# Optimization experiments

Measured on AMD Instinct MI355X. Metric: run time of the kernel, lower is better.

The kernel has to match this reference:

```python
import jax, jax.numpy as jnp
import numpy as np


def setup_inputs() -> dict:
    key = jax.random.key(0)
    k0, k1, k2, k3 = jax.random.split(key, 4)
    U, I, D, E = 100000, 50000, 128, 300000
    user_emb = jax.random.normal(k0, (U, D), dtype=jnp.float32) * 0.1
    item_emb = jax.random.normal(k1, (I, D), dtype=jnp.float32) * 0.1
    ui_src = jax.random.randint(k2, (E,), 0, U)          # user ids
    ui_dst = jax.random.randint(k3, (E,), 0, I)          # item ids
    # reverse ('item','rev_rates','user') edges are the transpose of the rating edges
    iu_src = ui_dst
    iu_dst = ui_src
    return {
        "user_emb": user_emb,
        "item_emb": item_emb,
        "ui_src": ui_src,
        "ui_dst": ui_dst,
        "iu_src": iu_src,
        "iu_dst": iu_dst,
        "num_users": U,
        "num_items": I,
        "num_layers": 2,
    }


def reference(user_emb, item_emb, ui_src, ui_dst, iu_src, iu_dst,
              num_users, num_items, num_layers):
    # Build homogeneous graph: item ids offset by num_users (as in encode()).
    N = num_users + num_items
    src = jnp.concatenate([ui_src, iu_src + num_users])        # [2E]
    dst = jnp.concatenate([ui_dst + num_users, iu_dst])        # [2E]
    x = jnp.concatenate([user_emb, item_emb], axis=0)          # [N, D]

    # gcn_norm without self-loops (PyG LGConv default): deg from in-edges.
    ones = jnp.ones(src.shape, dtype=x.dtype)
    deg = jax.ops.segment_sum(ones, dst, num_segments=N)       # [N]
    deg_inv_sqrt = jnp.where(deg > 0, 1.0 / jnp.sqrt(jnp.maximum(deg, 1.0)), 0.0)
    norm = deg_inv_sqrt[src] * deg_inv_sqrt[dst]               # [2E]

    # LightGCN: propagate num_layers times, average all layer outputs
    # (dropout is identity in eval mode).
    acc = x
    for _ in range(num_layers):
        x = jax.ops.segment_sum(x[src] * norm[:, None], dst, num_segments=N)
        acc = acc + x
    final = acc / (num_layers + 1)
    return final[:num_users], final[num_users:]
```

## Files before the change

kernel.cpp:

```cpp
#include <hip/hip_runtime.h>
#include <hip/hip_bf16.h>


#define DIM 128

struct __align__(8) Pair { int s; float w; };

__device__ __forceinline__ ushort f2bf(float f) {
    uint u = __float_as_uint(f);
    u += 0x7fffu + ((u >> 16) & 1u);
    return (ushort)(u >> 16);
}
__device__ __forceinline__ float bflo(uint u) { return __uint_as_float(u << 16); }
__device__ __forceinline__ float bfhi(uint u) { return __uint_as_float(u & 0xffff0000u); }

__global__ void deg_kernel(const int* __restrict__ ui_dst,
                           const int* __restrict__ iu_dst,
                           int E, int U, int* __restrict__ deg) {
    int e = blockIdx.x * blockDim.x + threadIdx.x;
    if (e < E) {
        atomicAdd(&deg[ui_dst[e] + U], 1);
        atomicAdd(&deg[iu_dst[e]], 1);
    }
}

__device__ __forceinline__ int block_incl_scan(int v, int* lds) {
    int lane = threadIdx.x & 63;
    int wid = threadIdx.x >> 6;
    int nw = (blockDim.x + 63) >> 6;
    #pragma unroll
    for (int off = 1; off < 64; off <<= 1) {
        int t = __shfl_up(v, off);
        if (lane >= off) v += t;
    }
    if (lane == 63) lds[wid] = v;
    __syncthreads();
    if (threadIdx.x == 0) {
        int s = 0;
        for (int w = 0; w < nw; w++) { int t = lds[w]; lds[w] = s; s += t; }
    }
    __syncthreads();
    return v + lds[wid];
}

__global__ void scan_partial_kernel(const int* __restrict__ deg, int N,
                                    int* __restrict__ partials) {
    __shared__ int lds[16];
    int i = blockIdx.x * 256 + threadIdx.x;
    int v = (i < N) ? deg[i] : 0;
    int incl = block_incl_scan(v, lds);
    if (threadIdx.x == 255) partials[blockIdx.x] = incl;
}

__global__ void scan_top_kernel(int* __restrict__ partials, int P,
                                int* __restrict__ row_ptr, int N) {
    __shared__ int lds[16];
    int i = threadIdx.x;
    int v = (i < P) ? partials[i] : 0;
    int incl = block_incl_scan(v, lds);
    if (i < P) partials[i] = incl - v;
    if (i == (int)blockDim.x - 1) row_ptr[N] = incl;
}

__global__ void scan_final_kernel(const int* __restrict__ deg, int N,
                                  const int* __restrict__ partials,
                                  int* __restrict__ row_ptr,
                                  int* __restrict__ cursor,
                                  float* __restrict__ dinv) {
    __shared__ int lds[16];
    int i = blockIdx.x * 256 + threadIdx.x;
    int v = (i < N) ? deg[i] : 0;
    int incl = block_incl_scan(v, lds);
    if (i < N) {
        int excl = incl - v + partials[blockIdx.x];
        row_ptr[i] = excl;
        cursor[i] = excl;
        dinv[i] = (v > 0) ? (1.0f / sqrtf((float)v)) : 0.0f;
    }
}

__global__ void fill_kernel(const int* __restrict__ ui_src,
                            const int* __restrict__ ui_dst,
                            const int* __restrict__ iu_src,
                            const int* __restrict__ iu_dst,
                            const float* __restrict__ dinv,
                            int E, int U,
                            int* __restrict__ cursor, Pair* __restrict__ pairs) {
    int e = blockIdx.x * blockDim.x + threadIdx.x;
    if (e >= E) return;
    int s = ui_src[e], d = ui_dst[e] + U;
    int pos = atomicAdd(&cursor[d], 1);
    pairs[pos] = {s, dinv[s]};
    s = iu_src[e] + U; d = iu_dst[e];
    pos = atomicAdd(&cursor[d], 1);
    pairs[pos] = {s, dinv[s]};
}

__global__ void convert_kernel(const float* __restrict__ xu,
                               const float* __restrict__ xi,
                               long uelems, long total,
                               ushort* __restrict__ xb) {
    long i8 = ((long)blockIdx.x * blockDim.x + threadIdx.x) * 8;
    if (i8 >= total) return;
    const float* src = (i8 < uelems) ? (xu + i8) : (xi + (i8 - uelems));
    float4 a = *reinterpret_cast<const float4*>(src);
    float4 b = *reinterpret_cast<const float4*>(src + 4);
    uint4 q;
    q.x = ((uint)f2bf(a.y) << 16) | f2bf(a.x);
    q.y = ((uint)f2bf(a.w) << 16) | f2bf(a.z);
    q.z = ((uint)f2bf(b.y) << 16) | f2bf(b.x);
    q.w = ((uint)f2bf(b.w) << 16) | f2bf(b.z);
    *reinterpret_cast<uint4*>(xb + i8) = q;
}

__global__ __launch_bounds__(256) void gather1_kernel(
        const ushort* __restrict__ xb,
        const int* __restrict__ row_ptr, const Pair* __restrict__ pairs,
        const float* __restrict__ dinv, int N, ushort* __restrict__ Tb) {
    long gt = (long)blockIdx.x * blockDim.x + threadIdx.x;
    int lane = (int)(gt & 15);
    long node = gt >> 4;
    if (node >= N) return;
    int start = row_ptr[node], end = row_ptr[node + 1];
    float a0 = 0.f, a1 = 0.f, a2 = 0.f, a3 = 0.f, a4 = 0.f, a5 = 0.f, a6 = 0.f, a7 = 0.f;
    int j = start;
    for (; j + 2 <= end; j += 2) {
        Pair p0 = pairs[j], p1 = pairs[j + 1];
        uint4 q0 = *reinterpret_cast<const uint4*>(xb + (size_t)p0.s * DIM + lane * 8);
        uint4 q1 = *reinterpret_cast<const uint4*>(xb + (size_t)p1.s * DIM + lane * 8);
        a0 = fmaf(bflo(q0.x), p0.w, fmaf(bflo(q1.x), p1.w, a0));
        a1 = fmaf(bfhi(q0.x), p0.w, fmaf(bfhi(q1.x), p1.w, a1));
        a2 = fmaf(bflo(q0.y), p0.w, fmaf(bflo(q1.y), p1.w, a2));
        a3 = fmaf(bfhi(q0.y), p0.w, fmaf(bfhi(q1.y), p1.w, a3));
        a4 = fmaf(bflo(q0.z), p0.w, fmaf(bflo(q1.z), p1.w, a4));
        a5 = fmaf(bfhi(q0.z), p0.w, fmaf(bfhi(q1.z), p1.w, a5));
        a6 = fmaf(bflo(q0.w), p0.w, fmaf(bflo(q1.w), p1.w, a6));
        a7 = fmaf(bfhi(q0.w), p0.w, fmaf(bfhi(q1.w), p1.w, a7));
    }
    if (j < end) {
        Pair p = pairs[j];
        uint4 q = *reinterpret_cast<const uint4*>(xb + (size_t)p.s * DIM + lane * 8);
        a0 = fmaf(bflo(q.x), p.w, a0);
        a1 = fmaf(bfhi(q.x), p.w, a1);
        a2 = fmaf(bflo(q.y), p.w, a2);
        a3 = fmaf(bfhi(q.y), p.w, a3);
        a4 = fmaf(bflo(q.z), p.w, a4);
        a5 = fmaf(bfhi(q.z), p.w, a5);
        a6 = fmaf(bflo(q.w), p.w, a6);
        a7 = fmaf(bfhi(q.w), p.w, a7);
    }
    float dd = dinv[node];
    uint4 r;
    r.x = ((uint)f2bf(a1 * dd) << 16) | f2bf(a0 * dd);
    r.y = ((uint)f2bf(a3 * dd) << 16) | f2bf(a2 * dd);
    r.z = ((uint)f2bf(a5 * dd) << 16) | f2bf(a4 * dd);
    r.w = ((uint)f2bf(a7 * dd) << 16) | f2bf(a6 * dd);
    *reinterpret_cast<uint4*>(Tb + (size_t)node * DIM + lane * 8) = r;
}

__global__ __launch_bounds__(256) void gather2_kernel(
        const float* __restrict__ xu, const float* __restrict__ xi,
        const ushort* __restrict__ Tb,
        const int* __restrict__ row_ptr, const Pair* __restrict__ pairs,
        const float* __restrict__ dinv, int N, int U, float* __restrict__ out) {
    long gt = (long)blockIdx.x * blockDim.x + threadIdx.x;
    int lane = (int)(gt & 15);
    long node = gt >> 4;
    if (node >= N) return;
    int start = row_ptr[node], end = row_ptr[node + 1];
    float a0 = 0.f, a1 = 0.f, a2 = 0.f, a3 = 0.f, a4 = 0.f, a5 = 0.f, a6 = 0.f, a7 = 0.f;
    int j = start;
    for (; j + 2 <= end; j += 2) {
        Pair p0 = pairs[j], p1 = pairs[j + 1];
        uint4 q0 = *reinterpret_cast<const uint4*>(Tb + (size_t)p0.s * DIM + lane * 8);
        uint4 q1 = *reinterpret_cast<const uint4*>(Tb + (size_t)p1.s * DIM + lane * 8);
        a0 = fmaf(bflo(q0.x), p0.w, fmaf(bflo(q1.x), p1.w, a0));
        a1 = fmaf(bfhi(q0.x), p0.w, fmaf(bfhi(q1.x), p1.w, a1));
        a2 = fmaf(bflo(q0.y), p0.w, fmaf(bflo(q1.y), p1.w, a2));
        a3 = fmaf(bfhi(q0.y), p0.w, fmaf(bfhi(q1.y), p1.w, a3));
        a4 = fmaf(bflo(q0.z), p0.w, fmaf(bflo(q1.z), p1.w, a4));
        a5 = fmaf(bfhi(q0.z), p0.w, fmaf(bfhi(q1.z), p1.w, a5));
        a6 = fmaf(bflo(q0.w), p0.w, fmaf(bflo(q1.w), p1.w, a6));
        a7 = fmaf(bfhi(q0.w), p0.w, fmaf(bfhi(q1.w), p1.w, a7));
    }
    if (j < end) {
        Pair p = pairs[j];
        uint4 q = *reinterpret_cast<const uint4*>(Tb + (size_t)p.s * DIM + lane * 8);
        a0 = fmaf(bflo(q.x), p.w, a0);
        a1 = fmaf(bfhi(q.x), p.w, a1);
        a2 = fmaf(bflo(q.y), p.w, a2);
        a3 = fmaf(bfhi(q.y), p.w, a3);
        a4 = fmaf(bflo(q.z), p.w, a4);
        a5 = fmaf(bfhi(q.z), p.w, a5);
        a6 = fmaf(bflo(q.w), p.w, a6);
        a7 = fmaf(bfhi(q.w), p.w, a7);
    }
    float dd = dinv[node];
    size_t off = (size_t)node * DIM + lane * 8;
    uint4 tq = *reinterpret_cast<const uint4*>(Tb + off);
    const float* x0p = (node < (long)U) ? (xu + off) : (xi + off - (size_t)U * DIM);
    float4 xa = *reinterpret_cast<const float4*>(x0p);
    float4 xc = *reinterpret_cast<const float4*>(x0p + 4);
    const float k = 1.0f / 3.0f;
    float4 r0, r1;
    r0.x = (xa.x + bflo(tq.x) + a0 * dd) * k;
    r0.y = (xa.y + bfhi(tq.x) + a1 * dd) * k;
    r0.z = (xa.z + bflo(tq.y) + a2 * dd) * k;
    r0.w = (xa.w + bfhi(tq.y) + a3 * dd) * k;
    r1.x = (xc.x + bflo(tq.z) + a4 * dd) * k;
    r1.y = (xc.y + bfhi(tq.z) + a5 * dd) * k;
    r1.z = (xc.z + bflo(tq.w) + a6 * dd) * k;
    r1.w = (xc.w + bfhi(tq.w) + a7 * dd) * k;
    *reinterpret_cast<float4*>(out + off) = r0;
    *reinterpret_cast<float4*>(out + off + 4) = r1;
}

extern "C" void kernel_launch(void* const* d_in, const int* in_sizes, int n_in,
                              void* d_out, int out_size, void* d_ws, size_t ws_size,
                              hipStream_t stream) {
    const float* user_emb = (const float*)d_in[0];
    const float* item_emb = (const float*)d_in[1];
    const int* ui_src = (const int*)d_in[2];
    const int* ui_dst = (const int*)d_in[3];
    const int* iu_src = (const int*)d_in[4];
    const int* iu_dst = (const int*)d_in[5];

    const int E = in_sizes[2];
    const int U = in_sizes[0] / DIM;
    const int I = in_sizes[1] / DIM;
    const int N = U + I;
    const int twoE = 2 * E;
    const long uelems = (long)U * DIM;
    const long total = (long)N * DIM;

    float* out = (float*)d_out;

    char* ws = (char*)d_ws;
    size_t off = 0;
    int* deg = (int*)(ws + off); off += (size_t)N * 4;
    int* cursor = (int*)(ws + off); off += (size_t)N * 4;
    int* row_ptr = (int*)(ws + off); off += (size_t)(N + 1) * 4;
    int* partials = (int*)(ws + off); off += 1024 * 4;
    float* dinv = (float*)(ws + off); off += (size_t)N * 4;
    off = (off + 7) & ~(size_t)7;
    Pair* pairs = (Pair*)(ws + off); off += (size_t)twoE * 8;
    off = (off + 511) & ~(size_t)511;
    ushort* xb = (ushort*)(ws + off); off += (size_t)total * 2;
    off = (off + 511) & ~(size_t)511;
    ushort* Tb = (ushort*)(ws + off);

    const int nPartBlocks = (N + 255) / 256;

    hipMemsetAsync(deg, 0, (size_t)N * 4, stream);

    deg_kernel<<<(E + 255) / 256, 256, 0, stream>>>(ui_dst, iu_dst, E, U, deg);

    scan_partial_kernel<<<nPartBlocks, 256, 0, stream>>>(deg, N, partials);
    scan_top_kernel<<<1, 1024, 0, stream>>>(partials, nPartBlocks, row_ptr, N);
    scan_final_kernel<<<nPartBlocks, 256, 0, stream>>>(deg, N, partials,
                                                       row_ptr, cursor, dinv);

    fill_kernel<<<(E + 255) / 256, 256, 0, stream>>>(ui_src, ui_dst, iu_src, iu_dst,
                                                     dinv, E, U, cursor, pairs);

    {
        long cthreads = total / 8;
        int cblocks = (int)((cthreads + 255) / 256);
        convert_kernel<<<cblocks, 256, 0, stream>>>(user_emb, item_emb,
                                                    uelems, total, xb);
    }

    {
        long threads = (long)N * 16;
        int blocks = (int)((threads + 255) / 256);
        gather1_kernel<<<blocks, 256, 0, stream>>>(xb, row_ptr, pairs, dinv, N, Tb);
        gather2_kernel<<<blocks, 256, 0, stream>>>(user_emb, item_emb, Tb,
                                                   row_ptr, pairs, dinv, N, U, out);
    }
}
```

Measured before the change: 292.4 us.

## Fuse all LightGCN stages into one cooperative persistent kernel with grid syncs

```diff
diff --git a/kernel.cpp b/kernel.cpp
--- a/kernel.cpp
+++ b/kernel.cpp
@@ -1,8 +1,13 @@
 #include <hip/hip_runtime.h>
+#include <hip/hip_cooperative_groups.h>
 #include <hip/hip_bf16.h>
 
+namespace cg = cooperative_groups;
+
 
 #define DIM 128
+#define NBLOCKS 1024
+#define NTHR 256
 
 struct __align__(8) Pair { int s; float w; };
 
@@ -14,20 +19,9 @@
 __device__ __forceinline__ float bflo(uint u) { return __uint_as_float(u << 16); }
 __device__ __forceinline__ float bfhi(uint u) { return __uint_as_float(u & 0xffff0000u); }
 
-__global__ void deg_kernel(const int* __restrict__ ui_dst,
-                           const int* __restrict__ iu_dst,
-                           int E, int U, int* __restrict__ deg) {
-    int e = blockIdx.x * blockDim.x + threadIdx.x;
-    if (e < E) {
-        atomicAdd(&deg[ui_dst[e] + U], 1);
-        atomicAdd(&deg[iu_dst[e]], 1);
-    }
-}
-
 __device__ __forceinline__ int block_incl_scan(int v, int* lds) {
     int lane = threadIdx.x & 63;
     int wid = threadIdx.x >> 6;
-    int nw = (blockDim.x + 63) >> 6;
     #pragma unroll
     for (int off = 1; off < 64; off <<= 1) {
         int t = __shfl_up(v, off);
@@ -37,200 +31,210 @@
     __syncthreads();
     if (threadIdx.x == 0) {
         int s = 0;
-        for (int w = 0; w < nw; w++) { int t = lds[w]; lds[w] = s; s += t; }
+        #pragma unroll
+        for (int w = 0; w < 4; w++) { int t = lds[w]; lds[w] = s; s += t; }
     }
     __syncthreads();
     return v + lds[wid];
 }
 
-__global__ void scan_partial_kernel(const int* __restrict__ deg, int N,
-                                    int* __restrict__ partials) {
+__global__ __launch_bounds__(256, 4) void lightgcn_all(
+        const float* __restrict__ xu, const float* __restrict__ xi,
+        const int* __restrict__ ui_src, const int* __restrict__ ui_dst,
+        const int* __restrict__ iu_src, const int* __restrict__ iu_dst,
+        int E, int U, int I,
+        int* __restrict__ deg, int* __restrict__ cursor,
+        int* __restrict__ row_ptr, int* __restrict__ partials,
+        float* __restrict__ dinv, Pair* __restrict__ pairs,
+        ushort* __restrict__ xb, ushort* __restrict__ Tb,
+        float* __restrict__ out) {
+    cg::grid_group grid = cg::this_grid();
     __shared__ int lds[16];
-    int i = blockIdx.x * 256 + threadIdx.x;
-    int v = (i < N) ? deg[i] : 0;
-    int incl = block_incl_scan(v, lds);
-    if (threadIdx.x == 255) partials[blockIdx.x] = incl;
-}
-
-__global__ void scan_top_kernel(int* __restrict__ partials, int P,
-                                int* __restrict__ row_ptr, int N) {
-    __shared__ int lds[16];
-    int i = threadIdx.x;
-    int v = (i < P) ? partials[i] : 0;
-    int incl = block_incl_scan(v, lds);
-    if (i < P) partials[i] = incl - v;
-    if (i == (int)blockDim.x - 1) row_ptr[N] = incl;
-}
-
-__global__ void scan_final_kernel(const int* __restrict__ deg, int N,
-                                  const int* __restrict__ partials,
-                                  int* __restrict__ row_ptr,
-                                  int* __restrict__ cursor,
-                                  float* __restrict__ dinv) {
-    __shared__ int lds[16];
-    int i = blockIdx.x * 256 + threadIdx.x;
-    int v = (i < N) ? deg[i] : 0;
-    int incl = block_incl_scan(v, lds);
-    if (i < N) {
-        int excl = incl - v + partials[blockIdx.x];
+    __shared__ int runsh;
+
+    const int N = U + I;
+    const long tid = (long)blockIdx.x * blockDim.x + threadIdx.x;
+    const long nth = (long)gridDim.x * blockDim.x;
+    const long total = (long)N * DIM;
+    const long uelems = (long)U * DIM;
+
+    for (long i = tid; i < N; i += nth) deg[i] = 0;
+    grid.sync();
+
+    for (long e = tid; e < E; e += nth) {
+        atomicAdd(&deg[ui_dst[e] + U], 1);
+        atomicAdd(&deg[iu_dst[e]], 1);
+    }
+    for (long u = tid; u < (total >> 3); u += nth) {
+        long i8 = u << 3;
+        const float* src = (i8 < uelems) ? (xu + i8) : (xi + (i8 - uelems));
+        float4 a = *reinterpret_cast<const float4*>(src);
+        float4 b = *reinterpret_cast<const float4*>(src + 4);
+        uint4 q;
+        q.x = ((uint)f2bf(a.y) << 16) | f2bf(a.x);
+        q.y = ((uint)f2bf(a.w) << 16) | f2bf(a.z);
+        q.z = ((uint)f2bf(b.y) << 16) | f2bf(b.x);
+        q.w = ((uint)f2bf(b.w) << 16) | f2bf(b.z);
+        *reinterpret_cast<uint4*>(xb + i8) = q;
+    }
+    grid.sync();
+
+    const int nchunk = (N + 255) >> 8;
+    for (int c = blockIdx.x; c < nchunk; c += gridDim.x) {
+        int i = (c << 8) + threadIdx.x;
+        int v = (i < N) ? deg[i] : 0;
+        int incl = block_incl_scan(v, lds);
+        if (i < N) row_ptr[i] = incl - v;
+        if (threadIdx.x == 255) partials[c] = incl;
+        __syncthreads();
+    }
+    grid.sync();
+
+    if (blockIdx.x == 0) {
+        if (threadIdx.x == 0) runsh = 0;
+        __syncthreads();
+        for (int base = 0; base < nchunk; base += 256) {
+            int idx = base + threadIdx.x;
+            int v = (idx < nchunk) ? partials[idx] : 0;
+            int incl = block_incl_scan(v, lds);
+            int run = runsh;
+            __syncthreads();
+            if (idx < nchunk) partials[idx] = incl - v + run;
+            if (threadIdx.x == 255) runsh = run + incl;
+            __syncthreads();
+        }
+        if (threadIdx.x == 0) row_ptr[N] = runsh;
+    }
+    grid.sync();
+
+    for (long i = tid; i < N; i += nth) {
+        int excl = row_ptr[i] + partials[i >> 8];
         row_ptr[i] = excl;
         cursor[i] = excl;
-        dinv[i] = (v > 0) ? (1.0f / sqrtf((float)v)) : 0.0f;
-    }
-}
-
-__global__ void fill_kernel(const int* __restrict__ ui_src,
-                            const int* __restrict__ ui_dst,
-                            const int* __restrict__ iu_src,
-                            const int* __restrict__ iu_dst,
-                            const float* __restrict__ dinv,
-                            int E, int U,
-                            int* __restrict__ cursor, Pair* __restrict__ pairs) {
-    int e = blockIdx.x * blockDim.x + threadIdx.x;
-    if (e >= E) return;
-    int s = ui_src[e], d = ui_dst[e] + U;
-    int pos = atomicAdd(&cursor[d], 1);
-    pairs[pos] = {s, dinv[s]};
-    s = iu_src[e] + U; d = iu_dst[e];
-    pos = atomicAdd(&cursor[d], 1);
-    pairs[pos] = {s, dinv[s]};
-}
-
-__global__ void convert_kernel(const float* __restrict__ xu,
-                               const float* __restrict__ xi,
-                               long uelems, long total,
-                               ushort* __restrict__ xb) {
-    long i8 = ((long)blockIdx.x * blockDim.x + threadIdx.x) * 8;
-    if (i8 >= total) return;
-    const float* src = (i8 < uelems) ? (xu + i8) : (xi + (i8 - uelems));
-    float4 a = *reinterpret_cast<const float4*>(src);
-    float4 b = *reinterpret_cast<const float4*>(src + 4);
-    uint4 q;
-    q.x = ((uint)f2bf(a.y) << 16) | f2bf(a.x);
-    q.y = ((uint)f2bf(a.w) << 16) | f2bf(a.z);
-    q.z = ((uint)f2bf(b.y) << 16) | f2bf(b.x);
-    q.w = ((uint)f2bf(b.w) << 16) | f2bf(b.z);
-    *reinterpret_cast<uint4*>(xb + i8) = q;
-}
-
-__global__ __launch_bounds__(256) void gather1_kernel(
-        const ushort* __restrict__ xb,
-        const int* __restrict__ row_ptr, const Pair* __restrict__ pairs,
-        const float* __restrict__ dinv, int N, ushort* __restrict__ Tb) {
-    long gt = (long)blockIdx.x * blockDim.x + threadIdx.x;
-    int lane = (int)(gt & 15);
-    long node = gt >> 4;
-    if (node >= N) return;
-    int start = row_ptr[node], end = row_ptr[node + 1];
-    float a0 = 0.f, a1 = 0.f, a2 = 0.f, a3 = 0.f, a4 = 0.f, a5 = 0.f, a6 = 0.f, a7 = 0.f;
-    int j = start;
-    for (; j + 2 <= end; j += 2) {
-        Pair p0 = pairs[j], p1 = pairs[j + 1];
-        uint4 q0 = *reinterpret_cast<const uint4*>(xb + (size_t)p0.s * DIM + lane * 8);
-        uint4 q1 = *reinterpret_cast<const uint4*>(xb + (size_t)p1.s * DIM + lane * 8);
-        a0 = fmaf(bflo(q0.x), p0.w, fmaf(bflo(q1.x), p1.w, a0));
-        a1 = fmaf(bfhi(q0.x), p0.w, fmaf(bfhi(q1.x), p1.w, a1));
-        a2 = fmaf(bflo(q0.y), p0.w, fmaf(bflo(q1.y), p1.w, a2));
-        a3 = fmaf(bfhi(q0.y), p0.w, fmaf(bfhi(q1.y), p1.w, a3));
-        a4 = fmaf(bflo(q0.z), p0.w, fmaf(bflo(q1.z), p1.w, a4));
-        a5 = fmaf(bfhi(q0.z), p0.w, fmaf(bfhi(q1.z), p1.w, a5));
-        a6 = fmaf(bflo(q0.w), p0.w, fmaf(bflo(q1.w), p1.w, a6));
-        a7 = fmaf(bfhi(q0.w), p0.w, fmaf(bfhi(q1.w), p1.w, a7));
-    }
-    if (j < end) {
-        Pair p = pairs[j];
-        uint4 q = *reinterpret_cast<const uint4*>(xb + (size_t)p.s * DIM + lane * 8);
-        a0 = fmaf(bflo(q.x), p.w, a0);
-        a1 = fmaf(bfhi(q.x), p.w, a1);
-        a2 = fmaf(bflo(q.y), p.w, a2);
-        a3 = fmaf(bfhi(q.y), p.w, a3);
-        a4 = fmaf(bflo(q.z), p.w, a4);
-        a5 = fmaf(bfhi(q.z), p.w, a5);
-        a6 = fmaf(bflo(q.w), p.w, a6);
-        a7 = fmaf(bfhi(q.w), p.w, a7);
-    }
-    float dd = dinv[node];
-    uint4 r;
-    r.x = ((uint)f2bf(a1 * dd) << 16) | f2bf(a0 * dd);
-    r.y = ((uint)f2bf(a3 * dd) << 16) | f2bf(a2 * dd);
-    r.z = ((uint)f2bf(a5 * dd) << 16) | f2bf(a4 * dd);
-    r.w = ((uint)f2bf(a7 * dd) << 16) | f2bf(a6 * dd);
-    *reinterpret_cast<uint4*>(Tb + (size_t)node * DIM + lane * 8) = r;
-}
-
-__global__ __launch_bounds__(256) void gather2_kernel(
-        const float* __restrict__ xu, const float* __restrict__ xi,
-        const ushort* __restrict__ Tb,
-        const int* __restrict__ row_ptr, const Pair* __restrict__ pairs,
-        const float* __restrict__ dinv, int N, int U, float* __restrict__ out) {
-    long gt = (long)blockIdx.x * blockDim.x + threadIdx.x;
-    int lane = (int)(gt & 15);
-    long node = gt >> 4;
-    if (node >= N) return;
-    int start = row_ptr[node], end = row_ptr[node + 1];
-    float a0 = 0.f, a1 = 0.f, a2 = 0.f, a3 = 0.f, a4 = 0.f, a5 = 0.f, a6 = 0.f, a7 = 0.f;
-    int j = start;
-    for (; j + 2 <= end; j += 2) {
-        Pair p0 = pairs[j], p1 = pairs[j + 1];
-        uint4 q0 = *reinterpret_cast<const uint4*>(Tb + (size_t)p0.s * DIM + lane * 8);
-        uint4 q1 = *reinterpret_cast<const uint4*>(Tb + (size_t)p1.s * DIM + lane * 8);
-        a0 = fmaf(bflo(q0.x), p0.w, fmaf(bflo(q1.x), p1.w, a0));
-        a1 = fmaf(bfhi(q0.x), p0.w, fmaf(bfhi(q1.x), p1.w, a1));
-        a2 = fmaf(bflo(q0.y), p0.w, fmaf(bflo(q1.y), p1.w, a2));
-        a3 = fmaf(bfhi(q0.y), p0.w, fmaf(bfhi(q1.y), p1.w, a3));
-        a4 = fmaf(bflo(q0.z), p0.w, fmaf(bflo(q1.z), p1.w, a4));
-        a5 = fmaf(bfhi(q0.z), p0.w, fmaf(bfhi(q1.z), p1.w, a5));
-        a6 = fmaf(bflo(q0.w), p0.w, fmaf(bflo(q1.w), p1.w, a6));
-        a7 = fmaf(bfhi(q0.w), p0.w, fmaf(bfhi(q1.w), p1.w, a7));
-    }
-    if (j < end) {
-        Pair p = pairs[j];
-        uint4 q = *reinterpret_cast<const uint4*>(Tb + (size_t)p.s * DIM + lane * 8);
-        a0 = fmaf(bflo(q.x), p.w, a0);
-        a1 = fmaf(bfhi(q.x), p.w, a1);
-        a2 = fmaf(bflo(q.y), p.w, a2);
-        a3 = fmaf(bfhi(q.y), p.w, a3);
-        a4 = fmaf(bflo(q.z), p.w, a4);
-        a5 = fmaf(bfhi(q.z), p.w, a5);
-        a6 = fmaf(bflo(q.w), p.w, a6);
-        a7 = fmaf(bfhi(q.w), p.w, a7);
-    }
-    float dd = dinv[node];
-    size_t off = (size_t)node * DIM + lane * 8;
-    uint4 tq = *reinterpret_cast<const uint4*>(Tb + off);
-    const float* x0p = (node < (long)U) ? (xu + off) : (xi + off - (size_t)U * DIM);
-    float4 xa = *reinterpret_cast<const float4*>(x0p);
-    float4 xc = *reinterpret_cast<const float4*>(x0p + 4);
-    const float k = 1.0f / 3.0f;
-    float4 r0, r1;
-    r0.x = (xa.x + bflo(tq.x) + a0 * dd) * k;
-    r0.y = (xa.y + bfhi(tq.x) + a1 * dd) * k;
-    r0.z = (xa.z + bflo(tq.y) + a2 * dd) * k;
-    r0.w = (xa.w + bfhi(tq.y) + a3 * dd) * k;
-    r1.x = (xc.x + bflo(tq.z) + a4 * dd) * k;
-    r1.y = (xc.y + bfhi(tq.z) + a5 * dd) * k;
-    r1.z = (xc.z + bflo(tq.w) + a6 * dd) * k;
-    r1.w = (xc.w + bfhi(tq.w) + a7 * dd) * k;
-    *reinterpret_cast<float4*>(out + off) = r0;
-    *reinterpret_cast<float4*>(out + off + 4) = r1;
+        int d = deg[i];
+        dinv[i] = (d > 0) ? rsqrtf((float)d) : 0.0f;
+    }
+    grid.sync();
+
+    for (long e = tid; e < E; e += nth) {
+        int s = ui_src[e], d0 = ui_dst[e] + U;
+        int pos = atomicAdd(&cursor[d0], 1);
+        pairs[pos] = {s, dinv[s]};
+        s = iu_src[e] + U; d0 = iu_dst[e];
+        pos = atomicAdd(&cursor[d0], 1);
+        pairs[pos] = {s, dinv[s]};
+    }
+    grid.sync();
+
+    const long lanes = (long)N * 16;
+    for (long u = tid; u < lanes; u += nth) {
+        int lane = (int)(u & 15);
+        long node = u >> 4;
+        int start = row_ptr[node], end = row_ptr[node + 1];
+        float a0 = 0.f, a1 = 0.f, a2 = 0.f, a3 = 0.f,
+              a4 = 0.f, a5 = 0.f, a6 = 0.f, a7 = 0.f;
+        int j = start;
+        for (; j + 2 <= end; j += 2) {
+            Pair p0 = pairs[j], p1 = pairs[j + 1];
+            uint4 q0 = *reinterpret_cast<const uint4*>(xb + (size_t)p0.s * DIM + lane * 8);
+            uint4 q1 = *reinterpret_cast<const uint4*>(xb + (size_t)p1.s * DIM + lane * 8);
+            a0 = fmaf(bflo(q0.x), p0.w, fmaf(bflo(q1.x), p1.w, a0));
+            a1 = fmaf(bfhi(q0.x), p0.w, fmaf(bfhi(q1.x), p1.w, a1));
+            a2 = fmaf(bflo(q0.y), p0.w, fmaf(bflo(q1.y), p1.w, a2));
+            a3 = fmaf(bfhi(q0.y), p0.w, fmaf(bfhi(q1.y), p1.w, a3));
+            a4 = fmaf(bflo(q0.z), p0.w, fmaf(bflo(q1.z), p1.w, a4));
+            a5 = fmaf(bfhi(q0.z), p0.w, fmaf(bfhi(q1.z), p1.w, a5));
+            a6 = fmaf(bflo(q0.w), p0.w, fmaf(bflo(q1.w), p1.w, a6));
+            a7 = fmaf(bfhi(q0.w), p0.w, fmaf(bfhi(q1.w), p1.w, a7));
+        }
+        if (j < end) {
+            Pair p = pairs[j];
+            uint4 q = *reinterpret_cast<const uint4*>(xb + (size_t)p.s * DIM + lane * 8);
+            a0 = fmaf(bflo(q.x), p.w, a0);
+            a1 = fmaf(bfhi(q.x), p.w, a1);
+            a2 = fmaf(bflo(q.y), p.w, a2);
+            a3 = fmaf(bfhi(q.y), p.w, a3);
+            a4 = fmaf(bflo(q.z), p.w, a4);
+            a5 = fmaf(bfhi(q.z), p.w, a5);
+            a6 = fmaf(bflo(q.w), p.w, a6);
+            a7 = fmaf(bfhi(q.w), p.w, a7);
+        }
+        float dd = dinv[node];
+        uint4 r;
+        r.x = ((uint)f2bf(a1 * dd) << 16) | f2bf(a0 * dd);
+        r.y = ((uint)f2bf(a3 * dd) << 16) | f2bf(a2 * dd);
+        r.z = ((uint)f2bf(a5 * dd) << 16) | f2bf(a4 * dd);
+        r.w = ((uint)f2bf(a7 * dd) << 16) | f2bf(a6 * dd);
+        *reinterpret_cast<uint4*>(Tb + (size_t)node * DIM + lane * 8) = r;
+    }
+    grid.sync();
+
+    for (long u = tid; u < lanes; u += nth) {
+        int lane = (int)(u & 15);
+        long node = u >> 4;
+        int start = row_ptr[node], end = row_ptr[node + 1];
+        float a0 = 0.f, a1 = 0.f, a2 = 0.f, a3 = 0.f,
+              a4 = 0.f, a5 = 0.f, a6 = 0.f, a7 = 0.f;
+        int j = start;
+        for (; j + 2 <= end; j += 2) {
+            Pair p0 = pairs[j], p1 = pairs[j + 1];
+            uint4 q0 = *reinterpret_cast<const uint4*>(Tb + (size_t)p0.s * DIM + lane * 8);
+            uint4 q1 = *reinterpret_cast<const uint4*>(Tb + (size_t)p1.s * DIM + lane * 8);
+            a0 = fmaf(bflo(q0.x), p0.w, fmaf(bflo(q1.x), p1.w, a0));
+            a1 = fmaf(bfhi(q0.x), p0.w, fmaf(bfhi(q1.x), p1.w, a1));
+            a2 = fmaf(bflo(q0.y), p0.w, fmaf(bflo(q1.y), p1.w, a2));
+            a3 = fmaf(bfhi(q0.y), p0.w, fmaf(bfhi(q1.y), p1.w, a3));
+            a4 = fmaf(bflo(q0.z), p0.w, fmaf(bflo(q1.z), p1.w, a4));
+            a5 = fmaf(bfhi(q0.z), p0.w, fmaf(bfhi(q1.z), p1.w, a5));
+            a6 = fmaf(bflo(q0.w), p0.w, fmaf(bflo(q1.w), p1.w, a6));
+            a7 = fmaf(bfhi(q0.w), p0.w, fmaf(bfhi(q1.w), p1.w, a7));
+        }
+        if (j < end) {
+            Pair p = pairs[j];
+            uint4 q = *reinterpret_cast<const uint4*>(Tb + (size_t)p.s * DIM + lane * 8);
+            a0 = fmaf(bflo(q.x), p.w, a0);
+            a1 = fmaf(bfhi(q.x), p.w, a1);
+            a2 = fmaf(bflo(q.y), p.w, a2);
+            a3 = fmaf(bfhi(q.y), p.w, a3);
+            a4 = fmaf(bflo(q.z), p.w, a4);
+            a5 = fmaf(bfhi(q.z), p.w, a5);
+            a6 = fmaf(bflo(q.w), p.w, a6);
+            a7 = fmaf(bfhi(q.w), p.w, a7);
+        }
+        float dd = dinv[node];
+        size_t off = (size_t)node * DIM + lane * 8;
+        uint4 tq = *reinterpret_cast<const uint4*>(Tb + off);
+        uint4 xq = *reinterpret_cast<const uint4*>(xb + off);
+        const float k = 1.0f / 3.0f;
+        float4 r0, r1;
+        r0.x = (bflo(xq.x) + bflo(tq.x) + a0 * dd) * k;
+        r0.y = (bfhi(xq.x) + bfhi(tq.x) + a1 * dd) * k;
+        r0.z = (bflo(xq.y) + bflo(tq.y) + a2 * dd) * k;
+        r0.w = (bfhi(xq.y) + bfhi(tq.y) + a3 * dd) * k;
+        r1.x = (bflo(xq.z) + bflo(tq.z) + a4 * dd) * k;
+        r1.y = (bfhi(xq.z) + bfhi(tq.z) + a5 * dd) * k;
+        r1.z = (bflo(xq.w) + bflo(tq.w) + a6 * dd) * k;
+        r1.w = (bfhi(xq.w) + bfhi(tq.w) + a7 * dd) * k;
+        *reinterpret_cast<float4*>(out + off) = r0;
+        *reinterpret_cast<float4*>(out + off + 4) = r1;
+    }
 }
 
 extern "C" void kernel_launch(void* const* d_in, const int* in_sizes, int n_in,
                               void* d_out, int out_size, void* d_ws, size_t ws_size,
                               hipStream_t stream) {
-    const float* user_emb = (const float*)d_in[0];
-    const float* item_emb = (const float*)d_in[1];
+    const float* xu = (const float*)d_in[0];
+    const float* xi = (const float*)d_in[1];
     const int* ui_src = (const int*)d_in[2];
     const int* ui_dst = (const int*)d_in[3];
     const int* iu_src = (const int*)d_in[4];
     const int* iu_dst = (const int*)d_in[5];
 
-    const int E = in_sizes[2];
-    const int U = in_sizes[0] / DIM;
-    const int I = in_sizes[1] / DIM;
+    int E = in_sizes[2];
+    int U = in_sizes[0] / DIM;
+    int I = in_sizes[1] / DIM;
     const int N = U + I;
     const int twoE = 2 * E;
-    const long uelems = (long)U * DIM;
     const long total = (long)N * DIM;
 
     float* out = (float*)d_out;
@@ -249,32 +253,13 @@
     off = (off + 511) & ~(size_t)511;
     ushort* Tb = (ushort*)(ws + off);
 
-    const int nPartBlocks = (N + 255) / 256;
-
-    hipMemsetAsync(deg, 0, (size_t)N * 4, stream);
-
-    deg_kernel<<<(E + 255) / 256, 256, 0, stream>>>(ui_dst, iu_dst, E, U, deg);
-
-    scan_partial_kernel<<<nPartBlocks, 256, 0, stream>>>(deg, N, partials);
-    scan_top_kernel<<<1, 1024, 0, stream>>>(partials, nPartBlocks, row_ptr, N);
-    scan_final_kernel<<<nPartBlocks, 256, 0, stream>>>(deg, N, partials,
-                                                       row_ptr, cursor, dinv);
-
-    fill_kernel<<<(E + 255) / 256, 256, 0, stream>>>(ui_src, ui_dst, iu_src, iu_dst,
-                                                     dinv, E, U, cursor, pairs);
-
-    {
-        long cthreads = total / 8;
-        int cblocks = (int)((cthreads + 255) / 256);
-        convert_kernel<<<cblocks, 256, 0, stream>>>(user_emb, item_emb,
-                                                    uelems, total, xb);
-    }
-
-    {
-        long threads = (long)N * 16;
-        int blocks = (int)((threads + 255) / 256);
-        gather1_kernel<<<blocks, 256, 0, stream>>>(xb, row_ptr, pairs, dinv, N, Tb);
-        gather2_kernel<<<blocks, 256, 0, stream>>>(user_emb, item_emb, Tb,
-                                                   row_ptr, pairs, dinv, N, U, out);
-    }
-}
+    void* args[] = {
+        (void*)&xu, (void*)&xi,
+        (void*)&ui_src, (void*)&ui_dst, (void*)&iu_src, (void*)&iu_dst,
+        (void*)&E, (void*)&U, (void*)&I,
+        (void*)&deg, (void*)&cursor, (void*)&row_ptr, (void*)&partials,
+        (void*)&dinv, (void*)&pairs, (void*)&xb, (void*)&Tb, (void*)&out
+    };
+    hipLaunchCooperativeKernel((void*)lightgcn_all, dim3(NBLOCKS), dim3(NTHR),
+                               args, 0, stream);
+}
```

After: 1.020 ms. 249% more time.
